# Kernel tuning notes

Hardware: AMD Instinct MI355X
Metric: run time of the kernel (lower is better)

The kernel has to match this reference:

```python
import jax, jax.numpy as jnp
import numpy as np

DIM, CTX_DIM, HEADS, HIDDEN = 1024, 768, 16, 4096
HEAD_DIM = DIM // HEADS
SCALE = HEAD_DIM ** -0.5


def _layernorm(x, w, b, eps=1e-5):
    mu = jnp.mean(x, axis=-1, keepdims=True)
    var = jnp.var(x, axis=-1, keepdims=True)
    return (x - mu) * jax.lax.rsqrt(var + eps) * w + b


def _heads(t):  # [B, L, H*D] -> [B, H, L, D]
    B, L, _ = t.shape
    return t.reshape(B, L, HEADS, HEAD_DIM).transpose(0, 2, 1, 3)


def _merge(t):  # [B, H, L, D] -> [B, L, H*D]
    B, H, L, D = t.shape
    return t.transpose(0, 2, 1, 3).reshape(B, L, H * D)


def _attn(xq, xkv, qw, qb, kw, kb, vw, vb, pw, pb):
    q = _heads(xq @ qw.T + qb)
    k = _heads(xkv @ kw.T + kb)
    v = _heads(xkv @ vw.T + vb)
    scores = jnp.einsum('bhld,bhsd->bhls', q, k) * SCALE
    probs = jax.nn.softmax(scores, axis=-1)
    out = _merge(jnp.einsum('bhls,bhsd->bhld', probs, v))
    return out @ pw.T + pb


def setup_inputs() -> dict:
    key = jax.random.key(0)
    ks = jax.random.split(key, 16)
    s = 0.02
    d = {
        'x': jax.random.normal(ks[0], (4, 2048, DIM), jnp.float32),
        'context': jax.random.normal(ks[1], (4, 77, CTX_DIM), jnp.float32),
        'ln1_w': jnp.ones((DIM,)), 'ln1_b': jnp.zeros((DIM,)),
        'ln2_w': jnp.ones((DIM,)), 'ln2_b': jnp.zeros((DIM,)),
        'ln3_w': jnp.ones((DIM,)), 'ln3_b': jnp.zeros((DIM,)),
        'sa_qw': jax.random.normal(ks[2], (DIM, DIM)) * s, 'sa_qb': jnp.zeros((DIM,)),
        'sa_kw': jax.random.normal(ks[3], (DIM, DIM)) * s, 'sa_kb': jnp.zeros((DIM,)),
        'sa_vw': jax.random.normal(ks[4], (DIM, DIM)) * s, 'sa_vb': jnp.zeros((DIM,)),
        'sa_pw': jax.random.normal(ks[5], (DIM, DIM)) * s, 'sa_pb': jnp.zeros((DIM,)),
        'ca_qw': jax.random.normal(ks[6], (DIM, DIM)) * s, 'ca_qb': jnp.zeros((DIM,)),
        'ca_kw': jax.random.normal(ks[7], (DIM, CTX_DIM)) * s, 'ca_kb': jnp.zeros((DIM,)),
        'ca_vw': jax.random.normal(ks[8], (DIM, CTX_DIM)) * s, 'ca_vb': jnp.zeros((DIM,)),
        'ca_pw': jax.random.normal(ks[9], (DIM, DIM)) * s, 'ca_pb': jnp.zeros((DIM,)),
        'fc1_w': jax.random.normal(ks[10], (HIDDEN, DIM)) * s, 'fc1_b': jnp.zeros((HIDDEN,)),
        'fc2_w': jax.random.normal(ks[11], (DIM, HIDDEN)) * s, 'fc2_b': jnp.zeros((DIM,)),
    }
    return d


def reference(x, context, ln1_w, ln1_b, ln2_w, ln2_b, ln3_w, ln3_b,
              sa_qw, sa_qb, sa_kw, sa_kb, sa_vw, sa_vb, sa_pw, sa_pb,
              ca_qw, ca_qb, ca_kw, ca_kb, ca_vw, ca_vb, ca_pw, ca_pb,
              fc1_w, fc1_b, fc2_w, fc2_b):
    h = _layernorm(x, ln1_w, ln1_b)
    x = x + _attn(h, h, sa_qw, sa_qb, sa_kw, sa_kb, sa_vw, sa_vb, sa_pw, sa_pb)
    h = _layernorm(x, ln2_w, ln2_b)
    x = x + _attn(h, context, ca_qw, ca_qb, ca_kw, ca_kb, ca_vw, ca_vb, ca_pw, ca_pb)
    h = _layernorm(x, ln3_w, ln3_b)
    h = jax.nn.gelu(h @ fc1_w.T + fc1_b, approximate=False)  # torch nn.GELU = exact
    x = x + (h @ fc2_w.T + fc2_b)
    return x
```

## Files before the change

kernel.cpp:

```cpp
#include <hip/hip_runtime.h>
#include <hip/hip_bf16.h>
#include <cstdint>
#include <cstddef>

typedef __attribute__((ext_vector_type(8))) short bf16x8;
typedef __attribute__((ext_vector_type(4))) float f32x4;
typedef __attribute__((ext_vector_type(16))) float f32x16;

__device__ __forceinline__ unsigned short f2bf(float f) {
  union { float f; unsigned u; } c; c.f = f;
  unsigned r = c.u + 0x7FFFu + ((c.u >> 16) & 1u);
  return (unsigned short)(r >> 16);
}

__device__ __forceinline__ unsigned cvtpk(float lo, float hi) {
  unsigned r;
  asm("v_cvt_pk_bf16_f32 %0, %1, %2" : "=v"(r) : "v"(lo), "v"(hi));
  return r;
}

__device__ __forceinline__ float gelu_fast(float v) {
  const float u = v * (0.7978845608f + 0.0356774081f * v * v);
  const float a = fminf(-2.8853900818f * u, 80.0f);
  return v / (1.0f + exp2f(a));
}

__device__ __forceinline__ int xcd_swz(int bid, int nwg) {
  const int cpx = nwg >> 3;
  return (bid & 7) * cpx + (bid >> 3);
}

typedef const __attribute__((address_space(1))) unsigned int* gas_ptr;
typedef __attribute__((address_space(3))) unsigned int* las_ptr;

__device__ __forceinline__ void gload16(const unsigned short* g, unsigned short* l) {
  __builtin_amdgcn_global_load_lds((gas_ptr)g, (las_ptr)l, 16, 0, 0);
}

struct WJ { const float* s; unsigned short* d; int nblk; };
struct WJobs { WJ j[10]; };

__global__ void wconv_k(WJobs jb) {
  const int bid = blockIdx.x;
  int base = 0, ji = -1;
  #pragma unroll
  for (int k = 0; k < 10; ++k) {
    const int nb = jb.j[k].nblk;
    if (ji < 0) { if (bid < base + nb) ji = k; else base += nb; }
  }
  const int i = (bid - base) * 256 + threadIdx.x;
  float4 v = ((const float4*)jb.j[ji].s)[i];
  ushort4 o;
  o.x = f2bf(v.x); o.y = f2bf(v.y); o.z = f2bf(v.z); o.w = f2bf(v.w);
  ((ushort4*)jb.j[ji].d)[i] = o;
}

__global__ void ctxpad_k(const float* __restrict__ ctx, unsigned short* __restrict__ out) {
  int i = blockIdx.x * blockDim.x + threadIdx.x;
  if (i >= 512 * 192) return;
  int r = i / 192, c4 = i % 192;
  int b = r >> 7, s = r & 127;
  ushort4 o = {0, 0, 0, 0};
  if (s < 77) {
    float4 v = ((const float4*)(ctx + (size_t)(b * 77 + s) * 768))[c4];
    o.x = f2bf(v.x); o.y = f2bf(v.y); o.z = f2bf(v.z); o.w = f2bf(v.w);
  }
  ((ushort4*)out)[i] = o;
}

__global__ __launch_bounds__(256)
void ln_k(const float* __restrict__ x, const float* __restrict__ w,
          const float* __restrict__ b, unsigned short* __restrict__ out) {
  int row = blockIdx.x, tid = threadIdx.x;
  float4 v = ((const float4*)(x + (size_t)row * 1024))[tid];
  float s = v.x + v.y + v.z + v.w;
  float s2 = v.x * v.x + v.y * v.y + v.z * v.z + v.w * v.w;
  #pragma unroll
  for (int m = 1; m < 64; m <<= 1) { s += __shfl_xor(s, m); s2 += __shfl_xor(s2, m); }
  __shared__ float ps[4], ps2[4];
  int wv = tid >> 6;
  if ((tid & 63) == 0) { ps[wv] = s; ps2[wv] = s2; }
  __syncthreads();
  s = ps[0] + ps[1] + ps[2] + ps[3];
  s2 = ps2[0] + ps2[1] + ps2[2] + ps2[3];
  float mu = s * (1.0f / 1024.0f);
  float var = s2 * (1.0f / 1024.0f) - mu * mu;
  float rstd = rsqrtf(var + 1e-5f);
  float4 wv4 = ((const float4*)w)[tid];
  float4 bv4 = ((const float4*)b)[tid];
  ushort4 o;
  o.x = f2bf((v.x - mu) * rstd * wv4.x + bv4.x);
  o.y = f2bf((v.y - mu) * rstd * wv4.y + bv4.y);
  o.z = f2bf((v.z - mu) * rstd * wv4.z + bv4.z);
  o.w = f2bf((v.w - mu) * rstd * wv4.w + bv4.w);
  ((ushort4*)(out + (size_t)row * 1024))[tid] = o;
}

#define SG_A(BUF, H, TE)                                                       \
  _Pragma("unroll")                                                            \
  for (int j = 0; j < AHL; ++j)                                                \
    __builtin_amdgcn_global_load_lds(                                          \
        (gas_ptr)(gA + (TE) + (size_t)((H) * (BM / 2) + j * 64) * (size_t)K),  \
        (las_ptr)(lds_all + (BUF) * AELEMS +                                   \
                  (((H) * (BM / 2) + j * 64) + w * 8) * 64),                   \
        16, 0, 0);

#define SG_B(BUF, H, TE)                                                       \
  _Pragma("unroll")                                                            \
  for (int j = 0; j < BHL; ++j)                                                \
    __builtin_amdgcn_global_load_lds(                                          \
        (gas_ptr)(gB + (TE) + (size_t)((H) * (BN / 2) + j * 64) * (size_t)K),  \
        (las_ptr)(lds_all + 2 * AELEMS + (BUF) * BELEMS +                      \
                  (((H) * (BN / 2) + j * 64) + w * 8) * 64),                   \
        16, 0, 0);

#define RD_A(MHh, BUF)                                                         \
  _Pragma("unroll")                                                            \
  for (int i = 0; i < MH; ++i) {                                               \
    const int r = ((MHh) * MH + i) * 32 + wr * 16 + ln;                        \
    _Pragma("unroll")                                                          \
    for (int kc = 0; kc < 2; ++kc)                                             \
      af[i][kc] = *(const bf16x8*)((const char*)lds_all + (BUF) * ABYTES +     \
                    r * 128 + (((kc * 4 + lg) ^ (r & 7)) * 16));               \
  }

#define RD_B(NHh, BUF)                                                         \
  _Pragma("unroll")                                                            \
  for (int i = 0; i < NIH; ++i) {                                              \
    const int ni = (NHh) * NIH + i;                                            \
    const int r = ni * 64 + wcc * 16 + ln;                                     \
    _Pragma("unroll")                                                          \
    for (int kc = 0; kc < 2; ++kc)                                             \
      bfr[ni][kc] = *(const bf16x8*)((const char*)lds_all + 2 * ABYTES +       \
                    (BUF) * BBYTES + r * 128 + (((kc * 4 + lg) ^ (r & 7)) * 16)); \
  }

#define QUAD(MHh, NHh)                                                         \
  __builtin_amdgcn_s_setprio(1);                                               \
  _Pragma("unroll")                                                            \
  for (int kc = 0; kc < 2; ++kc)                                               \
    _Pragma("unroll")                                                          \
    for (int i = 0; i < MH; ++i)                                               \
      _Pragma("unroll")                                                        \
      for (int j2 = 0; j2 < NIH; ++j2) {                                       \
        const int mi = (MHh) * MH + i, ni = (NHh) * NIH + j2;                  \
        if constexpr (SWAP)                                                    \
          acc[mi][ni] = __builtin_amdgcn_mfma_f32_16x16x32_bf16(               \
              bfr[ni][kc], af[i][kc], acc[mi][ni], 0, 0, 0);                   \
        else                                                                   \
          acc[mi][ni] = __builtin_amdgcn_mfma_f32_16x16x32_bf16(               \
              af[i][kc], bfr[ni][kc], acc[mi][ni], 0, 0, 0);                   \
      }                                                                        \
  __builtin_amdgcn_s_setprio(0);

#define VM_TILE()                                                              \
  do { if constexpr (BM == 256) asm volatile("s_waitcnt vmcnt(6)" ::: "memory"); \
       else                     asm volatile("s_waitcnt vmcnt(3)" ::: "memory"); } while (0)

#define TILE(BUF, TE)                                                          \
  {                                                                            \
    const int t = t2 + ((TE) / 64);                                            \
    RD_A(0, BUF) RD_B(0, BUF)                                                  \
    if (t + 1 < NT) { SG_B((BUF) ^ 1, 1, (TE) + 64) }                          \
    QUAD(0, 0)                                                                 \
    __builtin_amdgcn_s_barrier();                                              \
    RD_B(1, BUF)                                                               \
    if (t + 2 < NT) { SG_A(BUF, 0, (TE) + 128) }                               \
    QUAD(0, 1)                                                                 \
    __builtin_amdgcn_s_barrier();                                              \
    RD_A(1, BUF)                                                               \
    if (t + 2 < NT) { SG_B(BUF, 0, (TE) + 128) }                               \
    QUAD(1, 0)                                                                 \
    __builtin_amdgcn_s_barrier();                                              \
    if (t + 2 < NT) { SG_A(BUF, 1, (TE) + 128) }                               \
    QUAD(1, 1)                                                                 \
    if (t + 2 < NT) { VM_TILE(); }                                             \
    else            { asm volatile("s_waitcnt vmcnt(0)" ::: "memory"); }       \
    __builtin_amdgcn_s_barrier();                                              \
  }

template<int BM, int BN, int EPI, int SWAP, int MINW>
__global__ __launch_bounds__(512, MINW)
void gemm8(const unsigned short* __restrict__ A, const unsigned short* __restrict__ Bw,
           const float* __restrict__ bias0, const float* __restrict__ bias1,
           const float* __restrict__ res, void* __restrict__ C0, void* __restrict__ C1,
           int M, int N, int K, float scale0, int nsplit, int vtL) {
  (void)M;
  constexpr int MI = BM / 32;
  constexpr int MH = MI / 2;
  constexpr int AHL = BM / 128;
  constexpr int NI = BN / 64;
  constexpr int NIH = NI / 2;
  constexpr int BHL = BN / 128;
  constexpr int AELEMS = BM * 64;
  constexpr int BELEMS = BN * 64;
  constexpr int ABYTES = AELEMS * 2;
  constexpr int BBYTES = BELEMS * 2;
  __shared__ unsigned short lds_all[2 * AELEMS + 2 * BELEMS];

  const int tid = threadIdx.x;
  const int w = tid >> 6, lane = tid & 63;
  const int wr = w >> 2, wcc = w & 3;
  const int ln = lane & 15, lg = lane >> 4;
  const int nbn = N / BN;
  const int bid = xcd_swz(blockIdx.x, gridDim.x);
  const int bm = bid / nbn, bn = bid % nbn;
  const int NT = K >> 6;

  const int crow = tid >> 3;
  const int cslot = (tid & 7) ^ (crow & 7);

  const unsigned short* gA = A + ((size_t)(bm * BM) + crow) * K + cslot * 8;
  const unsigned short* gB = Bw + ((size_t)(bn * BN) + crow) * K + cslot * 8;

  bf16x8 af[MH][2], bfr[NI][2];
  f32x4 acc[MI][NI] = {};

  SG_A(0, 0, 0) SG_B(0, 0, 0) SG_B(0, 1, 0) SG_A(0, 1, 0)
  if (NT > 1) { SG_A(1, 0, 64) SG_B(1, 0, 64) SG_A(1, 1, 64) }
  VM_TILE();
  __builtin_amdgcn_s_barrier();

  for (int t2 = 0; t2 < NT; t2 += 2) {
    TILE(0, 0)
    TILE(1, 64)
    gA += 128; gB += 128;
  }

  const int rowbase = bm * BM + wr * 16;
  const int colbase = bn * BN + wcc * 16;
  if constexpr (EPI == 1) {
    #pragma unroll
    for (int ni = 0; ni < NI; ++ni) {
      const int col = colbase + ni * 64 + ln;
      const float bv = bias0[col];
      const int hh = col >> 6, dd = col & 63;
      #pragma unroll
      for (int mi = 0; mi < MI; ++mi) {
        const int row0 = rowbase + mi * 32 + lg * 4;
        const int bb = row0 / vtL, ss = row0 % vtL;
        ushort4 pk;
        pk.x = f2bf(acc[mi][ni][0] + bv);
        pk.y = f2bf(acc[mi][ni][1] + bv);
        pk.z = f2bf(acc[mi][ni][2] + bv);
        pk.w = f2bf(acc[mi][ni][3] + bv);
        *(ushort4*)((unsigned short*)C0 + ((size_t)((bb * 16 + hh) * 64 + dd)) * vtL + ss) = pk;
      }
    }
  } else {
    #pragma unroll
    for (int ni = 0; ni < NI; ++ni) {
      const int n0 = colbase + ni * 64 + lg * 4;
      const bool lo = (n0 < nsplit);
      const float* bp = lo ? bias0 : bias1;
      const float sc = lo ? scale0 : 1.0f;
      const int nc = lo ? n0 : n0 - nsplit;
      const int ldc = lo ? nsplit : N - nsplit;
      void* Cp = lo ? C0 : C1;
      const float4 b4 = *(const float4*)(bp + nc);
      #pragma unroll
      for (int mi = 0; mi < MI; ++mi) {
        const size_t mrow = (size_t)rowbase + mi * 32 + ln;
        float v0 = acc[mi][ni][0] + b4.x;
        float v1 = acc[mi][ni][1] + b4.y;
        float v2 = acc[mi][ni][2] + b4.z;
        float v3 = acc[mi][ni][3] + b4.w;
        if constexpr (EPI == 0) {
          ushort4 pk;
          pk.x = f2bf(v0 * sc); pk.y = f2bf(v1 * sc);
          pk.z = f2bf(v2 * sc); pk.w = f2bf(v3 * sc);
          *(ushort4*)((unsigned short*)Cp + mrow * ldc + nc) = pk;
        } else if constexpr (EPI == 2) {
          const float4 r4 = *(const float4*)(res + mrow * ldc + nc);
          float4 o4 = { v0 + r4.x, v1 + r4.y, v2 + r4.z, v3 + r4.w };
          *(float4*)((float*)Cp + mrow * ldc + nc) = o4;
        } else {
          ushort4 pk;
          pk.x = f2bf(gelu_fast(v0)); pk.y = f2bf(gelu_fast(v1));
          pk.z = f2bf(gelu_fast(v2)); pk.w = f2bf(gelu_fast(v3));
          *(ushort4*)((unsigned short*)Cp + mrow * ldc + nc) = pk;
        }
      }
    }
  }
}

__global__ __launch_bounds__(256, 2)
void flash_k(const unsigned short* __restrict__ Q, const unsigned short* __restrict__ Kg,
             const unsigned short* __restrict__ VT, unsigned short* __restrict__ O,
             int Lq, int Lkpad, int kvlen) {
  const int qblocks = Lq >> 8;
  const int bid = xcd_swz(blockIdx.x, gridDim.x);
  const int bh = bid / qblocks, qb = bid - bh * qblocks;
  const int b = bh >> 4, h = bh & 15;
  const int tid = threadIdx.x, w = tid >> 6, lane = tid & 63;
  const int l31 = lane & 31, hi = lane >> 5;

  __shared__ unsigned short Ks[2][64 * 64];
  __shared__ unsigned short Vs[2][64 * 64];

  const size_t qrow0 = (size_t)b * Lq + qb * 256 + w * 64 + l31;
  bf16x8 qf[2][4];
  #pragma unroll
  for (int u = 0; u < 2; ++u)
    #pragma unroll
    for (int ds = 0; ds < 4; ++ds)
      qf[u][ds] = *(const bf16x8*)(Q + (qrow0 + u * 32) * 1024 + h * 64 + ds * 16 + hi * 8);

  f32x16 oacc[2][2] = {};
  f32x4 lacc[2] = {};

  const int nst = (kvlen + 63) >> 6;
  const int srow = lane >> 3;
  const int gslot = (lane & 7) ^ srow;

  auto STAGE = [&](int buf, int st) {
    #pragma unroll
    for (int i = 0; i < 2; ++i) {
      const int r = i * 32 + w * 8 + srow;
      gload16(Kg + ((size_t)b * Lkpad + st * 64 + r) * 1024 + h * 64 + gslot * 8,
              &Ks[buf][(i * 32 + w * 8) * 64]);
      gload16(VT + ((size_t)bh * 64 + r) * Lkpad + (size_t)st * 64 + gslot * 8,
              &Vs[buf][(i * 32 + w * 8) * 64]);
    }
  };

  STAGE(0, 0);

  for (int st = 0; st < nst; ++st) {
    const int cur = st & 1;
    __syncthreads();
    if (st + 1 < nst) STAGE(cur ^ 1, st + 1);

    const char* Kb = (const char*)Ks[cur];
    const char* Vb = (const char*)Vs[cur];

    #pragma unroll
    for (int kb = 0; kb < 2; ++kb) {
      f32x16 s[2] = {};
      {
        const int r = kb * 32 + l31;
        const int sw = (r & 7) << 4;
        __builtin_amdgcn_s_setprio(1);
        #pragma unroll
        for (int ds = 0; ds < 4; ++ds) {
          bf16x8 kf = *(const bf16x8*)(Kb + r * 128 + ((ds * 32 + hi * 16) ^ sw));
          s[0] = __builtin_amdgcn_mfma_f32_32x32x16_bf16(kf, qf[0][ds], s[0], 0, 0, 0);
          s[1] = __builtin_amdgcn_mfma_f32_32x32x16_bf16(kf, qf[1][ds], s[1], 0, 0, 0);
        }
        __builtin_amdgcn_s_setprio(0);
      }

      if (st * 64 + 64 > kvlen) {
        const int kbase = st * 64 + kb * 32 + hi * 4;
        #pragma unroll
        for (int u = 0; u < 2; ++u)
          #pragma unroll
          for (int r = 0; r < 16; ++r)
            if (kbase + (r & 3) + 8 * (r >> 2) >= kvlen) s[u][r] = -1e30f;
      }

      bf16x8 pf[2][2];
      #pragma unroll
      for (int u = 0; u < 2; ++u) {
        #pragma unroll
        for (int r = 0; r < 16; ++r) s[u][r] = __builtin_amdgcn_exp2f(s[u][r]);
        #pragma unroll
        for (int rq = 0; rq < 4; ++rq) {
          f32x4 t = { s[u][rq * 4 + 0], s[u][rq * 4 + 1], s[u][rq * 4 + 2], s[u][rq * 4 + 3] };
          lacc[u] += t;
        }
        #pragma unroll
        for (int m = 0; m < 2; ++m) {
          unsigned u0 = cvtpk(s[u][8 * m + 0], s[u][8 * m + 1]);
          unsigned u1 = cvtpk(s[u][8 * m + 2], s[u][8 * m + 3]);
          unsigned u2 = cvtpk(s[u][8 * m + 4], s[u][8 * m + 5]);
          unsigned u3 = cvtpk(s[u][8 * m + 6], s[u][8 * m + 7]);
          asm volatile("v_permlane32_swap_b32 %0, %1" : "+v"(u0), "+v"(u2));
          asm volatile("v_permlane32_swap_b32 %0, %1" : "+v"(u1), "+v"(u3));
          union { unsigned uu[4]; bf16x8 v; } fr;
          fr.uu[0] = u0; fr.uu[1] = u1; fr.uu[2] = u2; fr.uu[3] = u3;
          pf[u][m] = fr.v;
        }
      }

      {
        const int sw2 = (l31 & 7) << 4;
        __builtin_amdgcn_s_setprio(1);
        #pragma unroll
        for (int db = 0; db < 2; ++db) {
          const int r = db * 32 + l31;
          #pragma unroll
          for (int m = 0; m < 2; ++m) {
            bf16x8 vf = *(const bf16x8*)(Vb + r * 128 +
                          ((kb * 64 + m * 32 + hi * 16) ^ sw2));
            oacc[0][db] = __builtin_amdgcn_mfma_f32_32x32x16_bf16(vf, pf[0][m], oacc[0][db], 0, 0, 0);
            oacc[1][db] = __builtin_amdgcn_mfma_f32_32x32x16_bf16(vf, pf[1][m], oacc[1][db], 0, 0, 0);
          }
        }
        __builtin_amdgcn_s_setprio(0);
      }
    }
  }

  #pragma unroll
  for (int u = 0; u < 2; ++u) {
    float lt = lacc[u][0] + lacc[u][1] + lacc[u][2] + lacc[u][3];
    lt += __shfl_xor(lt, 32);
    const float inv = 1.0f / lt;
    const size_t q = qrow0 + u * 32;
    #pragma unroll
    for (int db = 0; db < 2; ++db)
      #pragma unroll
      for (int rg = 0; rg < 4; ++rg) {
        ushort4 pk;
        pk.x = f2bf(oacc[u][db][rg * 4 + 0] * inv);
        pk.y = f2bf(oacc[u][db][rg * 4 + 1] * inv);
        pk.z = f2bf(oacc[u][db][rg * 4 + 2] * inv);
        pk.w = f2bf(oacc[u][db][rg * 4 + 3] * inv);
        *(ushort4*)(O + q * 1024 + h * 64 + db * 32 + rg * 8 + hi * 4) = pk;
      }
  }
}

extern "C" void kernel_launch(void* const* d_in, const int* in_sizes, int n_in,
                              void* d_out, int out_size, void* d_ws, size_t ws_size,
                              hipStream_t stream) {
  (void)in_sizes; (void)n_in; (void)out_size; (void)ws_size;
  const float* x     = (const float*)d_in[0];
  const float* ctx   = (const float*)d_in[1];
  const float* ln1_w = (const float*)d_in[2];
  const float* ln1_b = (const float*)d_in[3];
  const float* ln2_w = (const float*)d_in[4];
  const float* ln2_b = (const float*)d_in[5];
  const float* ln3_w = (const float*)d_in[6];
  const float* ln3_b = (const float*)d_in[7];
  const float* sa_qw = (const float*)d_in[8];  const float* sa_qb = (const float*)d_in[9];
  const float* sa_kw = (const float*)d_in[10]; const float* sa_kb = (const float*)d_in[11];
  const float* sa_vw = (const float*)d_in[12]; const float* sa_vb = (const float*)d_in[13];
  const float* sa_pw = (const float*)d_in[14]; const float* sa_pb = (const float*)d_in[15];
  const float* ca_qw = (const float*)d_in[16]; const float* ca_qb = (const float*)d_in[17];
  const float* ca_kw = (const float*)d_in[18]; const float* ca_kb = (const float*)d_in[19];
  const float* ca_vw = (const float*)d_in[20]; const float* ca_vb = (const float*)d_in[21];
  const float* ca_pw = (const float*)d_in[22]; const float* ca_pb = (const float*)d_in[23];
  const float* fc1_w = (const float*)d_in[24]; const float* fc1_b = (const float*)d_in[25];
  const float* fc2_w = (const float*)d_in[26]; const float* fc2_b = (const float*)d_in[27];

  char* ws = (char*)d_ws;
  size_t o = 0;
  auto give = [&](size_t bytes) { size_t r = o; o += (bytes + 255) & ~(size_t)255; return r; };
  const size_t SQ = 1048576, SC = 786432, SF = 4194304;
  unsigned short* w_qk  = (unsigned short*)(ws + give(2 * SQ * 2));
  unsigned short* w_v   = (unsigned short*)(ws + give(SQ * 2));
  unsigned short* w_p   = (unsigned short*)(ws + give(SQ * 2));
  unsigned short* w_caq = (unsigned short*)(ws + give(SQ * 2));
  unsigned short* w_cak = (unsigned short*)(ws + give(SC * 2));
  unsigned short* w_cav = (unsigned short*)(ws + give(SC * 2));
  unsigned short* w_cap = (unsigned short*)(ws + give(SQ * 2));
  unsigned short* w_f1  = (unsigned short*)(ws + give(SF * 2));
  unsigned short* w_f2  = (unsigned short*)(ws + give(SF * 2));
  unsigned short* ctxb  = (unsigned short*)(ws + give(512 * 768 * 2));
  unsigned short* hbuf  = (unsigned short*)(ws + give(8192 * 1024 * 2));
  unsigned short* qbuf  = (unsigned short*)(ws + give(8192 * 1024 * 2));
  unsigned short* kbuf  = (unsigned short*)(ws + give(8192 * 1024 * 2));
  unsigned short* vtbuf = (unsigned short*)(ws + give(8192 * 1024 * 2));
  unsigned short* obuf  = (unsigned short*)(ws + give(8192 * 1024 * 2));
  float*          xc    = (float*)(ws + give(8192 * 1024 * 4));
  unsigned short* gbuf  = qbuf;

  const float QSCALE = 0.125f * 1.44269504088896341f;

  WJobs jb;
  jb.j[0] = { sa_qw, w_qk,      (int)(SQ / 1024) };
  jb.j[1] = { sa_kw, w_qk + SQ, (int)(SQ / 1024) };
  jb.j[2] = { sa_vw, w_v,       (int)(SQ / 1024) };
  jb.j[3] = { sa_pw, w_p,       (int)(SQ / 1024) };
  jb.j[4] = { ca_qw, w_caq,     (int)(SQ / 1024) };
  jb.j[5] = { ca_kw, w_cak,     (int)(SC / 1024) };
  jb.j[6] = { ca_vw, w_cav,     (int)(SC / 1024) };
  jb.j[7] = { ca_pw, w_cap,     (int)(SQ / 1024) };
  jb.j[8] = { fc1_w, w_f1,      (int)(SF / 1024) };
  jb.j[9] = { fc2_w, w_f2,      (int)(SF / 1024) };
  int totblk = 0;
  for (int k = 0; k < 10; ++k) totblk += jb.j[k].nblk;

  wconv_k<<<totblk, 256, 0, stream>>>(jb);
  ctxpad_k<<<384, 256, 0, stream>>>(ctx, ctxb);

  ln_k<<<8192, 256, 0, stream>>>(x, ln1_w, ln1_b, hbuf);
  gemm8<256, 256, 0, 1, 2><<<256, 512, 0, stream>>>(hbuf, w_qk, sa_qb, sa_kb, nullptr, qbuf, kbuf,
                                                    8192, 2048, 1024, QSCALE, 1024, 0);
  gemm8<128, 128, 1, 0, 4><<<512, 512, 0, stream>>>(hbuf, w_v, sa_vb, nullptr, nullptr, vtbuf, nullptr,
                                                    8192, 1024, 1024, 1.0f, 1024, 2048);
  flash_k<<<512, 256, 0, stream>>>(qbuf, kbuf, vtbuf, obuf, 2048, 2048, 2048);
  gemm8<128, 128, 2, 1, 4><<<512, 512, 0, stream>>>(obuf, w_p, sa_pb, nullptr, x, xc, nullptr,
                                                    8192, 1024, 1024, 1.0f, 1024, 0);

  ln_k<<<8192, 256, 0, stream>>>(xc, ln2_w, ln2_b, hbuf);
  gemm8<128, 128, 0, 1, 4><<<512, 512, 0, stream>>>(hbuf, w_caq, ca_qb, nullptr, nullptr, qbuf, nullptr,
                                                    8192, 1024, 1024, QSCALE, 1024, 0);
  gemm8<128, 128, 0, 1, 4><<<32, 512, 0, stream>>>(ctxb, w_cak, ca_kb, nullptr, nullptr, kbuf, nullptr,
                                                   512, 1024, 768, 1.0f, 1024, 0);
  gemm8<128, 128, 1, 0, 4><<<32, 512, 0, stream>>>(ctxb, w_cav, ca_vb, nullptr, nullptr, vtbuf, nullptr,
                                                   512, 1024, 768, 1.0f, 1024, 128);
  flash_k<<<512, 256, 0, stream>>>(qbuf, kbuf, vtbuf, obuf, 2048, 128, 77);
  gemm8<128, 128, 2, 1, 4><<<512, 512, 0, stream>>>(obuf, w_cap, ca_pb, nullptr, xc, xc, nullptr,
                                                    8192, 1024, 1024, 1.0f, 1024, 0);

  ln_k<<<8192, 256, 0, stream>>>(xc, ln3_w, ln3_b, hbuf);
  gemm8<256, 256, 3, 1, 2><<<512, 512, 0, stream>>>(hbuf, w_f1, fc1_b, nullptr, nullptr, gbuf, nullptr,
                                                    8192, 4096, 1024, 1.0f, 4096, 0);
  gemm8<128, 128, 2, 1, 4><<<512, 512, 0, stream>>>(gbuf, w_f2, fc2_b, nullptr, xc, d_out, nullptr,
                                                    8192, 1024, 4096, 1.0f, 1024, 0);
}
```

Baseline: 461.9 us.

## Software-pipeline LDS fragment reads in 128x128 GEMM and fuse cross-attn K/V GEMM

Adds a PIPE variant of the GEMM main loop that double-buffers the A fragments in registers. The next tile's first A/B fragments are read from LDS while the final MFMA quadrant of the current tile is still computing, with explicit lgkmcnt waits and sched barriers. The goal is to hide LDS read latency behind MFMA work in all the 128x128 GEMMs. Separately, the cross-attention K and V projections become one launch with a split epilogue (EPI 4) that writes K row-major and V transposed. This costs extra registers and more complex wait/barrier ordering, which could hurt occupancy or correctness.

New measurement: 455.2 us, median of 2. Within noise of the previous version (-1.5%).

```diff
diff --git a/kernel.cpp b/kernel.cpp
--- a/kernel.cpp
+++ b/kernel.cpp
@@ -114,13 +114,13 @@
                   (((H) * (BN / 2) + j * 64) + w * 8) * 64),                   \
         16, 0, 0);
 
-#define RD_A(MHh, BUF)                                                         \
+#define RD_A(D, MHh, BUF)                                                      \
   _Pragma("unroll")                                                            \
   for (int i = 0; i < MH; ++i) {                                               \
     const int r = ((MHh) * MH + i) * 32 + wr * 16 + ln;                        \
     _Pragma("unroll")                                                          \
     for (int kc = 0; kc < 2; ++kc)                                             \
-      af[i][kc] = *(const bf16x8*)((const char*)lds_all + (BUF) * ABYTES +     \
+      af[D][i][kc] = *(const bf16x8*)((const char*)lds_all + (BUF) * ABYTES +  \
                     r * 128 + (((kc * 4 + lg) ^ (r & 7)) * 16));               \
   }
 
@@ -135,7 +135,7 @@
                     (BUF) * BBYTES + r * 128 + (((kc * 4 + lg) ^ (r & 7)) * 16)); \
   }
 
-#define QUAD(MHh, NHh)                                                         \
+#define QUAD(D, MHh, NHh)                                                      \
   __builtin_amdgcn_s_setprio(1);                                               \
   _Pragma("unroll")                                                            \
   for (int kc = 0; kc < 2; ++kc)                                               \
@@ -146,40 +146,75 @@
         const int mi = (MHh) * MH + i, ni = (NHh) * NIH + j2;                  \
         if constexpr (SWAP)                                                    \
           acc[mi][ni] = __builtin_amdgcn_mfma_f32_16x16x32_bf16(               \
-              bfr[ni][kc], af[i][kc], acc[mi][ni], 0, 0, 0);                   \
+              bfr[ni][kc], af[D][i][kc], acc[mi][ni], 0, 0, 0);                \
         else                                                                   \
           acc[mi][ni] = __builtin_amdgcn_mfma_f32_16x16x32_bf16(               \
-              af[i][kc], bfr[ni][kc], acc[mi][ni], 0, 0, 0);                   \
+              af[D][i][kc], bfr[ni][kc], acc[mi][ni], 0, 0, 0);                \
       }                                                                        \
   __builtin_amdgcn_s_setprio(0);
 
-#define VM_TILE()                                                              \
+#define VM_PRO()                                                               \
   do { if constexpr (BM == 256) asm volatile("s_waitcnt vmcnt(6)" ::: "memory"); \
        else                     asm volatile("s_waitcnt vmcnt(3)" ::: "memory"); } while (0)
 
-#define TILE(BUF, TE)                                                          \
+#define LGK0()                                                                 \
+  asm volatile("s_waitcnt lgkmcnt(0)" ::: "memory");                           \
+  __builtin_amdgcn_sched_barrier(0);
+
+#define TILE_NP(BUF, TE)                                                       \
   {                                                                            \
     const int t = t2 + ((TE) / 64);                                            \
-    RD_A(0, BUF) RD_B(0, BUF)                                                  \
+    RD_A(0, 0, BUF) RD_B(0, BUF)                                               \
     if (t + 1 < NT) { SG_B((BUF) ^ 1, 1, (TE) + 64) }                          \
-    QUAD(0, 0)                                                                 \
+    QUAD(0, 0, 0)                                                              \
     __builtin_amdgcn_s_barrier();                                              \
     RD_B(1, BUF)                                                               \
     if (t + 2 < NT) { SG_A(BUF, 0, (TE) + 128) }                               \
-    QUAD(0, 1)                                                                 \
-    __builtin_amdgcn_s_barrier();                                              \
-    RD_A(1, BUF)                                                               \
+    QUAD(0, 0, 1)                                                              \
+    __builtin_amdgcn_s_barrier();                                              \
+    RD_A(0, 1, BUF)                                                            \
     if (t + 2 < NT) { SG_B(BUF, 0, (TE) + 128) }                               \
-    QUAD(1, 0)                                                                 \
+    QUAD(0, 1, 0)                                                              \
     __builtin_amdgcn_s_barrier();                                              \
     if (t + 2 < NT) { SG_A(BUF, 1, (TE) + 128) }                               \
-    QUAD(1, 1)                                                                 \
-    if (t + 2 < NT) { VM_TILE(); }                                             \
+    QUAD(0, 1, 1)                                                              \
+    if (t + 2 < NT) { VM_PRO(); }                                              \
     else            { asm volatile("s_waitcnt vmcnt(0)" ::: "memory"); }       \
     __builtin_amdgcn_s_barrier();                                              \
   }
 
-template<int BM, int BN, int EPI, int SWAP, int MINW>
+#define TILE_P(BUF, TE)                                                        \
+  {                                                                            \
+    const int t = t2 + ((TE) / 64);                                            \
+                    \
+    if (t + 1 < NT) { SG_B((BUF) ^ 1, 1, (TE) + 64) }                          \
+    LGK0()                                                                     \
+    RD_B(1, BUF)                                                               \
+    QUAD(0, 0, 0)                                                              \
+    __builtin_amdgcn_s_barrier();                                              \
+                     \
+    if (t + 2 < NT) { SG_A(BUF, 0, (TE) + 128) }                               \
+    LGK0()                                                                     \
+    RD_A(1, 1, BUF)                                                            \
+    QUAD(0, 0, 1)                                                              \
+    __builtin_amdgcn_s_barrier();                                              \
+       \
+    if (t + 2 < NT) { SG_B(BUF, 0, (TE) + 128) }                               \
+    LGK0()                                                                     \
+    QUAD(1, 1, 1)                                                              \
+    if (t + 2 < NT) { asm volatile("s_waitcnt vmcnt(2)" ::: "memory"); }       \
+    else            { asm volatile("s_waitcnt vmcnt(0)" ::: "memory"); }       \
+    __builtin_amdgcn_s_barrier();                                              \
+    __builtin_amdgcn_sched_barrier(0);                                         \
+    \
+    if (t + 1 < NT) { RD_A(0, 0, (BUF) ^ 1) }                                  \
+    QUAD(1, 1, 0)                                                              \
+    if (t + 1 < NT) { RD_B(0, (BUF) ^ 1) }                                     \
+    if (t + 2 < NT) { SG_A(BUF, 1, (TE) + 128) }                               \
+    __builtin_amdgcn_s_barrier();                                              \
+  }
+
+template<int BM, int BN, int EPI, int SWAP, int MINW, int PIPE>
 __global__ __launch_bounds__(512, MINW)
 void gemm8(const unsigned short* __restrict__ A, const unsigned short* __restrict__ Bw,
            const float* __restrict__ bias0, const float* __restrict__ bias1,
@@ -213,17 +248,21 @@
   const unsigned short* gA = A + ((size_t)(bm * BM) + crow) * K + cslot * 8;
   const unsigned short* gB = Bw + ((size_t)(bn * BN) + crow) * K + cslot * 8;
 
-  bf16x8 af[MH][2], bfr[NI][2];
+  bf16x8 af[PIPE ? 2 : 1][MH][2], bfr[NI][2];
   f32x4 acc[MI][NI] = {};
 
   SG_A(0, 0, 0) SG_B(0, 0, 0) SG_B(0, 1, 0) SG_A(0, 1, 0)
   if (NT > 1) { SG_A(1, 0, 64) SG_B(1, 0, 64) SG_A(1, 1, 64) }
-  VM_TILE();
+  VM_PRO();
   __builtin_amdgcn_s_barrier();
+  if constexpr (PIPE) {
+    __builtin_amdgcn_sched_barrier(0);
+    RD_A(0, 0, 0) RD_B(0, 0)
+  }
 
   for (int t2 = 0; t2 < NT; t2 += 2) {
-    TILE(0, 0)
-    TILE(1, 64)
+    if constexpr (PIPE) { TILE_P(0, 0) TILE_P(1, 64) }
+    else                { TILE_NP(0, 0) TILE_NP(1, 64) }
     gA += 128; gB += 128;
   }
 
@@ -245,6 +284,37 @@
         pk.z = f2bf(acc[mi][ni][2] + bv);
         pk.w = f2bf(acc[mi][ni][3] + bv);
         *(ushort4*)((unsigned short*)C0 + ((size_t)((bb * 16 + hh) * 64 + dd)) * vtL + ss) = pk;
+      }
+    }
+  } else if constexpr (EPI == 4) {
+    #pragma unroll
+    for (int ni = 0; ni < NI; ++ni) {
+      const int col = colbase + ni * 64 + ln;
+      if (col < nsplit) {
+        const float bv = bias0[col];
+        #pragma unroll
+        for (int mi = 0; mi < MI; ++mi) {
+          const int row0 = rowbase + mi * 32 + lg * 4;
+          #pragma unroll
+          for (int r = 0; r < 4; ++r)
+            ((unsigned short*)C0)[(size_t)(row0 + r) * nsplit + col] =
+                f2bf(acc[mi][ni][r] + bv);
+        }
+      } else {
+        const int vc = col - nsplit;
+        const float bv = bias1[vc];
+        const int hh = vc >> 6, dd = vc & 63;
+        #pragma unroll
+        for (int mi = 0; mi < MI; ++mi) {
+          const int row0 = rowbase + mi * 32 + lg * 4;
+          const int bb = row0 / vtL, ss = row0 % vtL;
+          ushort4 pk;
+          pk.x = f2bf(acc[mi][ni][0] + bv);
+          pk.y = f2bf(acc[mi][ni][1] + bv);
+          pk.z = f2bf(acc[mi][ni][2] + bv);
+          pk.w = f2bf(acc[mi][ni][3] + bv);
+          *(ushort4*)((unsigned short*)C1 + ((size_t)((bb * 16 + hh) * 64 + dd)) * vtL + ss) = pk;
+        }
       }
     }
   } else {
@@ -454,8 +524,7 @@
   unsigned short* w_v   = (unsigned short*)(ws + give(SQ * 2));
   unsigned short* w_p   = (unsigned short*)(ws + give(SQ * 2));
   unsigned short* w_caq = (unsigned short*)(ws + give(SQ * 2));
-  unsigned short* w_cak = (unsigned short*)(ws + give(SC * 2));
-  unsigned short* w_cav = (unsigned short*)(ws + give(SC * 2));
+  unsigned short* w_cakv= (unsigned short*)(ws + give(2 * SC * 2));
   unsigned short* w_cap = (unsigned short*)(ws + give(SQ * 2));
   unsigned short* w_f1  = (unsigned short*)(ws + give(SF * 2));
   unsigned short* w_f2  = (unsigned short*)(ws + give(SF * 2));
@@ -471,16 +540,16 @@
   const float QSCALE = 0.125f * 1.44269504088896341f;
 
   WJobs jb;
-  jb.j[0] = { sa_qw, w_qk,      (int)(SQ / 1024) };
-  jb.j[1] = { sa_kw, w_qk + SQ, (int)(SQ / 1024) };
-  jb.j[2] = { sa_vw, w_v,       (int)(SQ / 1024) };
-  jb.j[3] = { sa_pw, w_p,       (int)(SQ / 1024) };
-  jb.j[4] = { ca_qw, w_caq,     (int)(SQ / 1024) };
-  jb.j[5] = { ca_kw, w_cak,     (int)(SC / 1024) };
-  jb.j[6] = { ca_vw, w_cav,     (int)(SC / 1024) };
-  jb.j[7] = { ca_pw, w_cap,     (int)(SQ / 1024) };
-  jb.j[8] = { fc1_w, w_f1,      (int)(SF / 1024) };
-  jb.j[9] = { fc2_w, w_f2,      (int)(SF / 1024) };
+  jb.j[0] = { sa_qw, w_qk,           (int)(SQ / 1024) };
+  jb.j[1] = { sa_kw, w_qk + SQ,      (int)(SQ / 1024) };
+  jb.j[2] = { sa_vw, w_v,            (int)(SQ / 1024) };
+  jb.j[3] = { sa_pw, w_p,            (int)(SQ / 1024) };
+  jb.j[4] = { ca_qw, w_caq,          (int)(SQ / 1024) };
+  jb.j[5] = { ca_kw, w_cakv,         (int)(SC / 1024) };
+  jb.j[6] = { ca_vw, w_cakv + SC,    (int)(SC / 1024) };
+  jb.j[7] = { ca_pw, w_cap,          (int)(SQ / 1024) };
+  jb.j[8] = { fc1_w, w_f1,           (int)(SF / 1024) };
+  jb.j[9] = { fc2_w, w_f2,           (int)(SF / 1024) };
   int totblk = 0;
   for (int k = 0; k < 10; ++k) totblk += jb.j[k].nblk;
 
@@ -488,28 +557,26 @@
   ctxpad_k<<<384, 256, 0, stream>>>(ctx, ctxb);
 
   ln_k<<<8192, 256, 0, stream>>>(x, ln1_w, ln1_b, hbuf);
-  gemm8<256, 256, 0, 1, 2><<<256, 512, 0, stream>>>(hbuf, w_qk, sa_qb, sa_kb, nullptr, qbuf, kbuf,
-                                                    8192, 2048, 1024, QSCALE, 1024, 0);
-  gemm8<128, 128, 1, 0, 4><<<512, 512, 0, stream>>>(hbuf, w_v, sa_vb, nullptr, nullptr, vtbuf, nullptr,
-                                                    8192, 1024, 1024, 1.0f, 1024, 2048);
+  gemm8<256, 256, 0, 1, 2, 0><<<256, 512, 0, stream>>>(hbuf, w_qk, sa_qb, sa_kb, nullptr, qbuf, kbuf,
+                                                       8192, 2048, 1024, QSCALE, 1024, 0);
+  gemm8<128, 128, 1, 0, 4, 1><<<512, 512, 0, stream>>>(hbuf, w_v, sa_vb, nullptr, nullptr, vtbuf, nullptr,
+                                                       8192, 1024, 1024, 1.0f, 1024, 2048);
   flash_k<<<512, 256, 0, stream>>>(qbuf, kbuf, vtbuf, obuf, 2048, 2048, 2048);
-  gemm8<128, 128, 2, 1, 4><<<512, 512, 0, stream>>>(obuf, w_p, sa_pb, nullptr, x, xc, nullptr,
-                                                    8192, 1024, 1024, 1.0f, 1024, 0);
+  gemm8<128, 128, 2, 1, 4, 1><<<512, 512, 0, stream>>>(obuf, w_p, sa_pb, nullptr, x, xc, nullptr,
+                                                       8192, 1024, 1024, 1.0f, 1024, 0);
 
   ln_k<<<8192, 256, 0, stream>>>(xc, ln2_w, ln2_b, hbuf);
-  gemm8<128, 128, 0, 1, 4><<<512, 512, 0, stream>>>(hbuf, w_caq, ca_qb, nullptr, nullptr, qbuf, nullptr,
-                                                    8192, 1024, 1024, QSCALE, 1024, 0);
-  gemm8<128, 128, 0, 1, 4><<<32, 512, 0, stream>>>(ctxb, w_cak, ca_kb, nullptr, nullptr, kbuf, nullptr,
-                                                   512, 1024, 768, 1.0f, 1024, 0);
-  gemm8<128, 128, 1, 0, 4><<<32, 512, 0, stream>>>(ctxb, w_cav, ca_vb, nullptr, nullptr, vtbuf, nullptr,
-                                                   512, 1024, 768, 1.0f, 1024, 128);
+  gemm8<128, 128, 0, 1, 4, 1><<<512, 512, 0, stream>>>(hbuf, w_caq, ca_qb, nullptr, nullptr, qbuf, nullptr,
+                                                       8192, 1024, 1024, QSCALE, 1024, 0);
+  gemm8<128, 128, 4, 0, 4, 1><<<64, 512, 0, stream>>>(ctxb, w_cakv, ca_kb, ca_vb, nullptr, kbuf, vtbuf,
+                                                      512, 2048, 768, 1.0f, 1024, 128);
   flash_k<<<512, 256, 0, stream>>>(qbuf, kbuf, vtbuf, obuf, 2048, 128, 77);
-  gemm8<128, 128, 2, 1, 4><<<512, 512, 0, stream>>>(obuf, w_cap, ca_pb, nullptr, xc, xc, nullptr,
-                                                    8192, 1024, 1024, 1.0f, 1024, 0);
+  gemm8<128, 128, 2, 1, 4, 1><<<512, 512, 0, stream>>>(obuf, w_cap, ca_pb, nullptr, xc, xc, nullptr,
+                                                       8192, 1024, 1024, 1.0f, 1024, 0);
 
   ln_k<<<8192, 256, 0, stream>>>(xc, ln3_w, ln3_b, hbuf);
-  gemm8<256, 256, 3, 1, 2><<<512, 512, 0, stream>>>(hbuf, w_f1, fc1_b, nullptr, nullptr, gbuf, nullptr,
-                                                    8192, 4096, 1024, 1.0f, 4096, 0);
-  gemm8<128, 128, 2, 1, 4><<<512, 512, 0, stream>>>(gbuf, w_f2, fc2_b, nullptr, xc, d_out, nullptr,
-                                                    8192, 1024, 4096, 1.0f, 1024, 0);
-}
+  gemm8<256, 256, 3, 1, 2, 0><<<512, 512, 0, stream>>>(hbuf, w_f1, fc1_b, nullptr, nullptr, gbuf, nullptr,
+                                                       8192, 4096, 1024, 1.0f, 4096, 0);
+  gemm8<128, 128, 2, 1, 4, 1><<<512, 512, 0, stream>>>(gbuf, w_f2, fc2_b, nullptr, xc, d_out, nullptr,
+                                                       8192, 1024, 4096, 1.0f, 1024, 0);
+}
```
